# Optimization experiments

Hardware: AMD Instinct MI355X
Metric: run time of the kernel (lower is better)

The kernel has to match this reference:

```python
import jax, jax.numpy as jnp
import numpy as np

NUM_USERS = 1_000_000
NUM_ITEMS = 1_000_000
F = 64
B = 16384


def setup_inputs() -> dict:
    key = jax.random.key(0)
    k1, k2, k3, k4 = jax.random.split(key, 4)
    return {
        "user_indices": jax.random.randint(k1, (B,), 0, NUM_USERS),
        "item_indices": jax.random.randint(k2, (B,), 0, NUM_ITEMS),
        "user_factors": jax.random.normal(k3, (NUM_USERS, F), dtype=jnp.float32),
        "item_factors": jax.random.normal(k4, (NUM_ITEMS, F), dtype=jnp.float32),
    }


def reference(user_indices, item_indices, user_factors, item_factors):
    # torch: mm(user_emb, item_emb.T).sum(-1)
    # == user_emb @ sum_over_batch(item_emb)  (exact linear-algebra identity)
    u = user_factors[user_indices]            # [B, F] gather
    v = item_factors[item_indices]            # [B, F] gather
    # einsum contracts both c (item batch) and f, avoiding the [B, B] intermediate
    return jnp.einsum("bf,cf->b", u, v)       # [B]
```

## Files before the change

### kernel.cpp

```cpp
#include <hip/hip_runtime.h>
#include <hip/hip_bf16.h>


#define FDIM 64
#define NB1 64
#define NB2 512
#define NTHREADS 256
#define WPB 4
#define R1 16
#define R2 2

__global__ void __launch_bounds__(NTHREADS)
mf_item_sum(const int* __restrict__ item_idx,
            const float* __restrict__ item_factors,
            float* __restrict__ s_part, int B) {
    const int lane = threadIdx.x & 63;
    const int wid  = threadIdx.x >> 6;
    const int rg   = lane >> 4;
    const int fs   = lane & 15;
    const int waveBase = (blockIdx.x * WPB + wid) * (R1 * 4);

    int idx[R1];
    #pragma unroll
    for (int r = 0; r < R1; ++r) {
        const int p = waveBase + r * 4 + rg;
        idx[r] = (p < B) ? item_idx[p] : -1;
    }

    float4 acc = make_float4(0.f, 0.f, 0.f, 0.f);
    #pragma unroll
    for (int r = 0; r < R1; ++r) {
        if (idx[r] >= 0) {
            const float4 v = *(const float4*)(item_factors + (size_t)idx[r] * FDIM + fs * 4);
            acc.x += v.x; acc.y += v.y; acc.z += v.z; acc.w += v.w;
        }
    }

    #pragma unroll
    for (int m = 16; m <= 32; m <<= 1) {
        acc.x += __shfl_xor(acc.x, m);
        acc.y += __shfl_xor(acc.y, m);
        acc.z += __shfl_xor(acc.z, m);
        acc.w += __shfl_xor(acc.w, m);
    }

    __shared__ float4 red[WPB][16];
    if (lane < 16) red[wid][fs] = acc;
    __syncthreads();
    if (threadIdx.x < 16) {
        const float4 a = red[0][threadIdx.x], b = red[1][threadIdx.x],
                     c = red[2][threadIdx.x], d = red[3][threadIdx.x];
        float4 t;
        t.x = a.x + b.x + c.x + d.x;
        t.y = a.y + b.y + c.y + d.y;
        t.z = a.z + b.z + c.z + d.z;
        t.w = a.w + b.w + c.w + d.w;
        *(float4*)(s_part + blockIdx.x * FDIM + threadIdx.x * 4) = t;
    }
}

__global__ void __launch_bounds__(NTHREADS)
mf_user_dot(const int* __restrict__ user_idx,
            const float* __restrict__ user_factors,
            const float* __restrict__ s_part,
            float* __restrict__ out, int B) {
    const int lane = threadIdx.x & 63;
    const int wid  = threadIdx.x >> 6;
    const int rg   = lane >> 4;
    const int fs   = lane & 15;

    __shared__ float sred[4][FDIM];
    __shared__ float s_lds[FDIM];
    {
        const int f = threadIdx.x & 63;
        const int g = threadIdx.x >> 6;
        float p = 0.f;
        #pragma unroll
        for (int c = 0; c < NB1 / 4; ++c)
            p += s_part[(g * (NB1 / 4) + c) * FDIM + f];
        sred[g][f] = p;
    }
    __syncthreads();
    if (threadIdx.x < FDIM)
        s_lds[threadIdx.x] = sred[0][threadIdx.x] + sred[1][threadIdx.x] +
                             sred[2][threadIdx.x] + sred[3][threadIdx.x];
    __syncthreads();

    const float4 s4 = *(const float4*)(s_lds + fs * 4);

    const int waveBase = (blockIdx.x * WPB + wid) * (R2 * 4);
    #pragma unroll
    for (int r = 0; r < R2; ++r) {
        const int p = waveBase + r * 4 + rg;
        if (p < B) {
            const int u = user_idx[p];
            const float4 uv = *(const float4*)(user_factors + (size_t)u * FDIM + fs * 4);
            float v = uv.x * s4.x + uv.y * s4.y + uv.z * s4.z + uv.w * s4.w;
            v += __shfl_xor(v, 1);
            v += __shfl_xor(v, 2);
            v += __shfl_xor(v, 4);
            v += __shfl_xor(v, 8);
            if (fs == 0) out[p] = v;
        }
    }
}

extern "C" void kernel_launch(void* const* d_in, const int* in_sizes, int n_in,
                              void* d_out, int out_size, void* d_ws, size_t ws_size,
                              hipStream_t stream) {
    const int*   user_idx     = (const int*)d_in[0];
    const int*   item_idx     = (const int*)d_in[1];
    const float* user_factors = (const float*)d_in[2];
    const float* item_factors = (const float*)d_in[3];
    float*       out          = (float*)d_out;
    float*       s_part       = (float*)d_ws;
    const int B = in_sizes[0];

    mf_item_sum<<<NB1, NTHREADS, 0, stream>>>(item_idx, item_factors, s_part, B);
    mf_user_dot<<<NB2, NTHREADS, 0, stream>>>(user_idx, user_factors, s_part, out, B);
}
```

Before: 12.62 us.

## Spread item gather over more blocks and prefetch user rows before partial reduction

The item-sum kernel now runs with 256 blocks at 4 rows per lane group instead of 64 blocks at 16, so more waves issue random gathers concurrently. In the user-dot kernel, user indices and factor rows are loaded before the block reduces the partial sums. This lets the gather latency overlap the reduction and its barriers. The reduction is restructured as float4 loads over 256 partials with a two-level LDS reduction, which gives every user-dot block 4x more partial data to read.

```diff
diff --git a/kernel.cpp b/kernel.cpp
--- a/kernel.cpp
+++ b/kernel.cpp
@@ -3,11 +3,11 @@
 
 
 #define FDIM 64
-#define NB1 64
+#define NB1 256
 #define NB2 512
 #define NTHREADS 256
 #define WPB 4
-#define R1 16
+#define R1 4
 #define R2 2
 
 __global__ void __launch_bounds__(NTHREADS)
@@ -69,39 +69,55 @@
     const int rg   = lane >> 4;
     const int fs   = lane & 15;
 
-    __shared__ float sred[4][FDIM];
-    __shared__ float s_lds[FDIM];
+    const int waveBase = (blockIdx.x * WPB + wid) * (R2 * 4);
+    int p[R2], u[R2];
+    float4 uv[R2];
+    #pragma unroll
+    for (int r = 0; r < R2; ++r) {
+        p[r] = waveBase + r * 4 + rg;
+        u[r] = (p[r] < B) ? user_idx[p[r]] : -1;
+    }
+    #pragma unroll
+    for (int r = 0; r < R2; ++r)
+        uv[r] = (u[r] >= 0)
+            ? *(const float4*)(user_factors + (size_t)u[r] * FDIM + fs * 4)
+            : make_float4(0.f, 0.f, 0.f, 0.f);
+
+    const float4* s_part4 = (const float4*)s_part;
+    __shared__ float4 sred[16][16];
+    __shared__ float4 s_lds4[16];
     {
-        const int f = threadIdx.x & 63;
-        const int g = threadIdx.x >> 6;
-        float p = 0.f;
+        const int cg  = threadIdx.x >> 4;
+        const int sl  = threadIdx.x & 15;
+        float4 a = make_float4(0.f, 0.f, 0.f, 0.f);
         #pragma unroll
-        for (int c = 0; c < NB1 / 4; ++c)
-            p += s_part[(g * (NB1 / 4) + c) * FDIM + f];
-        sred[g][f] = p;
+        for (int j = 0; j < 16; ++j) {
+            const float4 v = s_part4[(cg * 16 + j) * 16 + sl];
+            a.x += v.x; a.y += v.y; a.z += v.z; a.w += v.w;
+        }
+        sred[cg][sl] = a;
     }
     __syncthreads();
-    if (threadIdx.x < FDIM)
-        s_lds[threadIdx.x] = sred[0][threadIdx.x] + sred[1][threadIdx.x] +
-                             sred[2][threadIdx.x] + sred[3][threadIdx.x];
+    if (threadIdx.x < 16) {
+        float4 a = make_float4(0.f, 0.f, 0.f, 0.f);
+        #pragma unroll
+        for (int j = 0; j < 16; ++j) {
+            const float4 v = sred[j][threadIdx.x];
+            a.x += v.x; a.y += v.y; a.z += v.z; a.w += v.w;
+        }
+        s_lds4[threadIdx.x] = a;
+    }
     __syncthreads();
+    const float4 s4 = s_lds4[fs];
 
-    const float4 s4 = *(const float4*)(s_lds + fs * 4);
-
-    const int waveBase = (blockIdx.x * WPB + wid) * (R2 * 4);
     #pragma unroll
     for (int r = 0; r < R2; ++r) {
-        const int p = waveBase + r * 4 + rg;
-        if (p < B) {
-            const int u = user_idx[p];
-            const float4 uv = *(const float4*)(user_factors + (size_t)u * FDIM + fs * 4);
-            float v = uv.x * s4.x + uv.y * s4.y + uv.z * s4.z + uv.w * s4.w;
-            v += __shfl_xor(v, 1);
-            v += __shfl_xor(v, 2);
-            v += __shfl_xor(v, 4);
-            v += __shfl_xor(v, 8);
-            if (fs == 0) out[p] = v;
-        }
+        float v = uv[r].x * s4.x + uv[r].y * s4.y + uv[r].z * s4.z + uv[r].w * s4.w;
+        v += __shfl_xor(v, 1);
+        v += __shfl_xor(v, 2);
+        v += __shfl_xor(v, 4);
+        v += __shfl_xor(v, 8);
+        if (fs == 0 && p[r] < B) out[p[r]] = v;
     }
 }
 
```

Result: slower. 13.49 us (+7.0%).
